# Kernel tuning notes

Measured on AMD Instinct MI355X. Metric: run time of the kernel, lower is better.

The kernel has to match this reference:

```python
import jax, jax.numpy as jnp
import numpy as np

D = 128  # embed dim

def linear(x, W, b):
    return x @ W.T + b

def mha1(x, w_in, b_in, w_out, b_out):
    # Single-head MultiheadAttention, x: (S, B, D), seq-first like torch.nn.MultiheadAttention
    q, k, v = jnp.split(x @ w_in.T + b_in, 3, axis=-1)
    scores = jnp.einsum('sbd,tbd->bst', q, k) / jnp.sqrt(jnp.asarray(D, x.dtype))
    att = jax.nn.softmax(scores, axis=-1)
    o = jnp.einsum('bst,tbd->sbd', att, v)
    return o @ w_out.T + b_out

def setup_inputs() -> dict:
    key = jax.random.key(0)
    ks = iter(jax.random.split(key, 32))
    def p(shape, scale=0.02):
        return (jax.random.normal(next(ks), shape, dtype=jnp.float32) * scale)
    B, S, F = 8, 2048, 3584
    inp = {
        'x': jax.random.normal(next(ks), (B, S, F), dtype=jnp.float32),
        'place_W': p((128, 2048)), 'place_b': p((128,)),
        'cast_W': p((128, 512)), 'cast_b': p((128,)),
        'action_W': p((128, 512)), 'action_b': p((128,)),
        'audio_W': p((128, 512)), 'audio_b': p((128,)),
        'e_W': p((128, 512)), 'e_b': p((128,)),
        'la_win': p((3 * D, D)), 'la_bin': p((3 * D,)),
        'la_wout': p((D, D)), 'la_bout': p((D,)),
        'be_W': p((128, 256)), 'be_b': p((128,)),
        'ba_win': p((3 * D, D)), 'ba_bin': p((3 * D,)),
        'ba_wout': p((D, D)), 'ba_bout': p((D,)),
        'bp_W': p((1, 128)), 'bp_b': p((1,)),
    }
    return inp

def reference(x, place_W, place_b, cast_W, cast_b, action_W, action_b,
              audio_W, audio_b, e_W, e_b, la_win, la_bin, la_wout, la_bout,
              be_W, be_b, ba_win, ba_bin, ba_wout, ba_bout, bp_W, bp_b):
    # --- forward_embeddings ---
    place = jax.nn.relu(linear(x[:, :, :2048], place_W, place_b))
    cast = jax.nn.relu(linear(x[:, :, 2048:2560], cast_W, cast_b))
    action = jax.nn.relu(linear(x[:, :, 2560:3072], action_W, action_b))
    audio = jax.nn.relu(linear(x[:, :, 3072:3584], audio_W, audio_b))
    feats = jnp.concatenate((place, cast, action, audio), axis=2)  # (B,S,512)
    e = jax.nn.relu(linear(feats, e_W, e_b))  # (B,S,128)
    e = jnp.transpose(e, (1, 0, 2))  # (S,B,128) seq-first
    e = mha1(e, la_win, la_bin, la_wout, la_bout)
    # --- forward_segmentation (single-pass prefix/suffix means) ---
    S = e.shape[0]
    csum = jnp.cumsum(e, axis=0)  # (S,B,D)
    total = csum[-1]
    i = jnp.arange(1, S, dtype=e.dtype)[:, None, None]
    left = csum[:-1] / i                       # mean of e[:i]
    right = (total[None] - csum[:-1]) / (S - i)  # mean of e[i:]
    cat = jnp.concatenate((left, right), axis=-1)  # (S-1,B,256)
    b = jax.nn.relu(linear(cat, be_W, be_b))
    b = mha1(b, ba_win, ba_bin, ba_wout, ba_bout)
    b = jax.nn.sigmoid(linear(b, bp_W, bp_b))[..., 0]  # (S-1,B)
    return (e, b)
```

## Files before the change

### kernel.cpp

```cpp
#include <hip/hip_runtime.h>
#include <hip/hip_bf16.h>
#include <math.h>
#include <stdint.h>


#define DEV static __device__ __forceinline__

typedef __attribute__((ext_vector_type(8))) short bf16x8;
typedef __attribute__((ext_vector_type(4))) float f32x4;

DEV uint32_t pk2bf(float a, float b) {
  __hip_bfloat162 h = __float22bfloat162_rn(make_float2(a, b));
  return *(uint32_t*)&h;
}
DEV uint2 cvt4(float4 f) {
  return make_uint2(pk2bf(f.x, f.y), pk2bf(f.z, f.w));
}
DEV uint16_t bf1(float a) { return (uint16_t)(pk2bf(a, 0.f) & 0xffffu); }
DEV float frombf(uint16_t h) {
  union { uint32_t u; float f; } v; v.u = ((uint32_t)h) << 16; return v.f;
}

#define WAIT_VM0()  __asm__ volatile("s_waitcnt vmcnt(0)" ::: "memory")
#define WAIT_LGKM0() __asm__ volatile("s_waitcnt lgkmcnt(0)" ::: "memory")
#define RAW_BARRIER() __builtin_amdgcn_s_barrier()

#define OFF_PW      0u
#define OFF_CW      262144u
#define OFF_AW      327680u
#define OFF_UW      393216u
#define OFF_EW      458752u
#define OFF_LAWIN   524288u
#define OFF_LAWOUT  573440u
#define OFF_BEW     589824u
#define OFF_BAWIN   622592u
#define OFF_BAWOUT  671744u
#define OFF_END     688128u

struct WPtrs { const float* p[10]; };

__global__ __launch_bounds__(256) void pack_weights(WPtrs wp, uint16_t* __restrict__ WB)
{
  const uint32_t off[11] = {OFF_PW, OFF_CW, OFF_AW, OFF_UW, OFF_EW, OFF_LAWIN,
                            OFF_LAWOUT, OFF_BEW, OFF_BAWIN, OFF_BAWOUT, OFF_END};
  uint32_t h = (blockIdx.x * 256u + threadIdx.x) * 4u;
  if (h >= OFF_END) return;
  int s = 0;
  while (h >= off[s + 1]) ++s;
  float4 f = *(const float4*)(wp.p[s] + (h - off[s]));
  *(uint2*)(WB + h) = cvt4(f);
}

template<bool ABF, bool OBF, bool RELU, bool REMAP>
__global__ __launch_bounds__(256) void gemm64(
    const void* __restrict__ Ap, int lda,
    const uint16_t* __restrict__ Wb,
    const float* __restrict__ bias,
    void* __restrict__ Cp, int ldc,
    int M, int K)
{
  __shared__ __align__(16) uint16_t As[64 * 72];
  __shared__ __align__(16) uint16_t Ws[128 * 72];

  const int t  = threadIdx.x;
  const int m0 = blockIdx.x * 64;
  const int n0 = blockIdx.y * 128;
  const int w  = t >> 6, l = t & 63;
  const int ln = l & 15, qd = l >> 4;

  f32x4 acc[4][2];
#pragma unroll
  for (int i = 0; i < 4; ++i) { acc[i][0] = (f32x4){0,0,0,0}; acc[i][1] = (f32x4){0,0,0,0}; }

  const int rr = t >> 4;
  const int cl = (t & 15) * 4;
  const int r8 = t >> 3;
  const int c8 = (t & 7) * 8;

  float4 a32[4];
  bf16x8 a16[2];
  bf16x8 wreg[4];

  auto loadA = [&](int k0) {
    if (ABF) {
      const uint16_t* A = (const uint16_t*)Ap;
#pragma unroll
      for (int i = 0; i < 2; ++i) {
        int m = m0 + r8 + 32 * i;
        int mc = m < M ? m : M - 1;
        a16[i] = *(const bf16x8*)(A + (size_t)mc * lda + k0 + c8);
      }
    } else {
      const float* A = (const float*)Ap;
#pragma unroll
      for (int i = 0; i < 4; ++i) {
        int m = m0 + rr + 16 * i;
        int mc = m < M ? m : M - 1;
        a32[i] = *(const float4*)(A + (size_t)mc * lda + k0 + cl);
      }
    }
#pragma unroll
    for (int i = 0; i < 4; ++i) {
      int n = r8 + 32 * i;
      wreg[i] = *(const bf16x8*)(Wb + (size_t)(n0 + n) * K + k0 + c8);
    }
  };
  auto writeLDS = [&]() {
    if (ABF) {
#pragma unroll
      for (int i = 0; i < 2; ++i)
        *(bf16x8*)(As + (size_t)(r8 + 32 * i) * 72 + c8) = a16[i];
    } else {
#pragma unroll
      for (int i = 0; i < 4; ++i)
        *(uint2*)(As + (size_t)(rr + 16 * i) * 72 + cl) = cvt4(a32[i]);
    }
#pragma unroll
    for (int i = 0; i < 4; ++i)
      *(bf16x8*)(Ws + (size_t)(r8 + 32 * i) * 72 + c8) = wreg[i];
  };

  loadA(0);
  for (int k0 = 0; k0 < K; k0 += 64) {
    WAIT_VM0();
    writeLDS();
    WAIT_LGKM0();
    RAW_BARRIER();
    if (k0 + 64 < K) loadA(k0 + 64);
#pragma unroll
    for (int ks = 0; ks < 2; ++ks) {
      bf16x8 af[4], bfr[2];
#pragma unroll
      for (int mf = 0; mf < 4; ++mf)
        af[mf] = *(const bf16x8*)(As + (size_t)(mf * 16 + ln) * 72 + ks * 32 + qd * 8);
#pragma unroll
      for (int nf = 0; nf < 2; ++nf)
        bfr[nf] = *(const bf16x8*)(Ws + (size_t)(w * 32 + nf * 16 + ln) * 72 + ks * 32 + qd * 8);
#pragma unroll
      for (int mf = 0; mf < 4; ++mf)
#pragma unroll
        for (int nf = 0; nf < 2; ++nf)
          acc[mf][nf] = __builtin_amdgcn_mfma_f32_16x16x32_bf16(af[mf], bfr[nf], acc[mf][nf], 0, 0, 0);
    }
    RAW_BARRIER();
  }

#pragma unroll
  for (int mf = 0; mf < 4; ++mf) {
#pragma unroll
    for (int r = 0; r < 4; ++r) {
      int m = m0 + mf * 16 + qd * 4 + r;
      if (m < M) {
        size_t ro = REMAP ? (size_t)((m & 2047) * 8 + (m >> 11)) : (size_t)m;
#pragma unroll
        for (int nf = 0; nf < 2; ++nf) {
          int n = n0 + w * 32 + nf * 16 + ln;
          float v = acc[mf][nf][r] + bias[n];
          if (RELU) v = fmaxf(v, 0.f);
          if (OBF) ((uint16_t*)Cp)[ro * (size_t)ldc + n] = bf1(v);
          else     ((float*)Cp)[ro * (size_t)ldc + n] = v;
        }
      }
    }
  }
}

__global__ __launch_bounds__(256) void gemm_feats64(
    const float* __restrict__ x, const uint16_t* __restrict__ WB,
    const float* __restrict__ pb, const float* __restrict__ cb,
    const float* __restrict__ ab, const float* __restrict__ ub,
    uint16_t* __restrict__ feats)
{
  __shared__ __align__(16) uint16_t As[64 * 72];
  __shared__ __align__(16) uint16_t Ws[128 * 72];

  const int seg = blockIdx.y;
  const uint16_t* Wb; const float* bias; int kbase, Kseg;
  if (seg == 0)      { Wb = WB + OFF_PW; bias = pb; kbase = 0;    Kseg = 2048; }
  else if (seg == 1) { Wb = WB + OFF_CW; bias = cb; kbase = 2048; Kseg = 512; }
  else if (seg == 2) { Wb = WB + OFF_AW; bias = ab; kbase = 2560; Kseg = 512; }
  else               { Wb = WB + OFF_UW; bias = ub; kbase = 3072; Kseg = 512; }

  const int t  = threadIdx.x;
  const int m0 = blockIdx.x * 64;
  const int w  = t >> 6, l = t & 63;
  const int ln = l & 15, qd = l >> 4;

  f32x4 acc[4][2];
#pragma unroll
  for (int i = 0; i < 4; ++i) { acc[i][0] = (f32x4){0,0,0,0}; acc[i][1] = (f32x4){0,0,0,0}; }

  const int rr = t >> 4;
  const int cl = (t & 15) * 4;
  const int r8 = t >> 3;
  const int c8 = (t & 7) * 8;

  float4 a32[4];
  bf16x8 wreg[4];

  auto loadA = [&](int k0) {
#pragma unroll
    for (int i = 0; i < 4; ++i) {
      int m = m0 + rr + 16 * i;
      a32[i] = *(const float4*)(x + (size_t)m * 3584 + kbase + k0 + cl);
    }
#pragma unroll
    for (int i = 0; i < 4; ++i) {
      int n = r8 + 32 * i;
      wreg[i] = *(const bf16x8*)(Wb + (size_t)n * Kseg + k0 + c8);
    }
  };

  loadA(0);
  for (int k0 = 0; k0 < Kseg; k0 += 64) {
    WAIT_VM0();
#pragma unroll
    for (int i = 0; i < 4; ++i)
      *(uint2*)(As + (size_t)(rr + 16 * i) * 72 + cl) = cvt4(a32[i]);
#pragma unroll
    for (int i = 0; i < 4; ++i)
      *(bf16x8*)(Ws + (size_t)(r8 + 32 * i) * 72 + c8) = wreg[i];
    WAIT_LGKM0();
    RAW_BARRIER();
    if (k0 + 64 < Kseg) loadA(k0 + 64);
#pragma unroll
    for (int ks = 0; ks < 2; ++ks) {
      bf16x8 af[4], bfr[2];
#pragma unroll
      for (int mf = 0; mf < 4; ++mf)
        af[mf] = *(const bf16x8*)(As + (size_t)(mf * 16 + ln) * 72 + ks * 32 + qd * 8);
#pragma unroll
      for (int nf = 0; nf < 2; ++nf)
        bfr[nf] = *(const bf16x8*)(Ws + (size_t)(w * 32 + nf * 16 + ln) * 72 + ks * 32 + qd * 8);
#pragma unroll
      for (int mf = 0; mf < 4; ++mf)
#pragma unroll
        for (int nf = 0; nf < 2; ++nf)
          acc[mf][nf] = __builtin_amdgcn_mfma_f32_16x16x32_bf16(af[mf], bfr[nf], acc[mf][nf], 0, 0, 0);
    }
    RAW_BARRIER();
  }

#pragma unroll
  for (int mf = 0; mf < 4; ++mf) {
#pragma unroll
    for (int r = 0; r < 4; ++r) {
      int m = m0 + mf * 16 + qd * 4 + r;
#pragma unroll
      for (int nf = 0; nf < 2; ++nf) {
        int n = w * 32 + nf * 16 + ln;
        float v = fmaxf(acc[mf][nf][r] + bias[n], 0.f);
        feats[(size_t)m * 512 + seg * 128 + n] = bf1(v);
      }
    }
  }
}

__global__ __launch_bounds__(256) void gemm_becat64(
    const float* __restrict__ csum, const float* __restrict__ part,
    const uint16_t* __restrict__ Wb, const float* __restrict__ bias,
    uint16_t* __restrict__ C)
{
  __shared__ __align__(16) uint16_t As[64 * 72];
  __shared__ __align__(16) uint16_t Ws[128 * 72];

  const int M = 16376, K = 256;
  const int t  = threadIdx.x;
  const int m0 = blockIdx.x * 64;
  const int w  = t >> 6, l = t & 63;
  const int ln = l & 15, qd = l >> 4;

  f32x4 acc[4][2];
#pragma unroll
  for (int i = 0; i < 4; ++i) { acc[i][0] = (f32x4){0,0,0,0}; acc[i][1] = (f32x4){0,0,0,0}; }

  const int rr = t >> 4;
  const int cl = (t & 15) * 4;
  const int r8 = t >> 3;
  const int c8 = (t & 7) * 8;

  for (int k0 = 0; k0 < K; k0 += 64) {
    __syncthreads();
#pragma unroll
    for (int i = 0; i < 4; ++i) {
      int m = m0 + rr + 16 * i;
      int mc = m < M ? m : M - 1;
      int j = mc >> 3, bb = mc & 7;
      int kk = k0 + cl;
      float4 f;
      if (kk < 128) {
        float4 v = *(const float4*)(csum + (size_t)mc * 128 + kk);
        float4 p = *(const float4*)(part + (size_t)(bb * 64 + (j >> 5)) * 128 + kk);
        float s = 1.f / (float)(j + 1);
        f = make_float4((v.x + p.x) * s, (v.y + p.y) * s,
                        (v.z + p.z) * s, (v.w + p.w) * s);
      } else {
        int d = kk - 128;
        float4 c0 = *(const float4*)(csum + (size_t)mc * 128 + d);
        float4 p0 = *(const float4*)(part + (size_t)(bb * 64 + (j >> 5)) * 128 + d);
        float4 ct = *(const float4*)(csum + (size_t)(16376 + bb) * 128 + d);
        float4 pt = *(const float4*)(part + (size_t)(bb * 64 + 63) * 128 + d);
        float s = 1.f / (float)(2047 - j);
        f = make_float4(((ct.x + pt.x) - (c0.x + p0.x)) * s,
                        ((ct.y + pt.y) - (c0.y + p0.y)) * s,
                        ((ct.z + pt.z) - (c0.z + p0.z)) * s,
                        ((ct.w + pt.w) - (c0.w + p0.w)) * s);
      }
      *(uint2*)(As + (size_t)(rr + 16 * i) * 72 + cl) = cvt4(f);
    }
#pragma unroll
    for (int i = 0; i < 4; ++i) {
      int n = r8 + 32 * i;
      *(bf16x8*)(Ws + (size_t)n * 72 + c8) =
          *(const bf16x8*)(Wb + (size_t)n * K + k0 + c8);
    }
    __syncthreads();
#pragma unroll
    for (int ks = 0; ks < 2; ++ks) {
      bf16x8 af[4], bfr[2];
#pragma unroll
      for (int mf = 0; mf < 4; ++mf)
        af[mf] = *(const bf16x8*)(As + (size_t)(mf * 16 + ln) * 72 + ks * 32 + qd * 8);
#pragma unroll
      for (int nf = 0; nf < 2; ++nf)
        bfr[nf] = *(const bf16x8*)(Ws + (size_t)(w * 32 + nf * 16 + ln) * 72 + ks * 32 + qd * 8);
#pragma unroll
      for (int mf = 0; mf < 4; ++mf)
#pragma unroll
        for (int nf = 0; nf < 2; ++nf)
          acc[mf][nf] = __builtin_amdgcn_mfma_f32_16x16x32_bf16(af[mf], bfr[nf], acc[mf][nf], 0, 0, 0);
    }
  }

#pragma unroll
  for (int mf = 0; mf < 4; ++mf) {
#pragma unroll
    for (int r = 0; r < 4; ++r) {
      int m = m0 + mf * 16 + qd * 4 + r;
      if (m < M) {
#pragma unroll
        for (int nf = 0; nf < 2; ++nf) {
          int n = w * 32 + nf * 16 + ln;
          C[(size_t)m * 128 + n] = bf1(fmaxf(acc[mf][nf][r] + bias[n], 0.f));
        }
      }
    }
  }
}

__global__ __launch_bounds__(256) void vpack(
    const uint16_t* __restrict__ proj, uint16_t* __restrict__ Vtb, int Slen)
{
  __shared__ __align__(16) uint16_t Vs[64][136];

  const int kt = blockIdx.x, b = blockIdx.y, t = threadIdx.x;
  const int sl = t >> 2, cg = (t & 3) * 32;
  const int s  = kt * 64 + sl;
  const int valid = s < Slen;
  const int sc2 = valid ? s : Slen - 1;
  const uint16_t* src = proj + ((size_t)sc2 * 8 + b) * 384 + 256 + cg;
#pragma unroll
  for (int i = 0; i < 4; ++i) {
    bf16x8 v;
    if (valid) v = *(const bf16x8*)(src + i * 8);
    else       v = (bf16x8){0,0,0,0,0,0,0,0};
    *(bf16x8*)(&Vs[sl][cg + i * 8]) = v;
  }
  __syncthreads();
  const int d = t >> 1, hh = t & 1;
  uint32_t wv[16];
#pragma unroll
  for (int i = 0; i < 16; ++i) {
    int K = 32 * hh + 16 * ((i >> 1) & 1) + 4 * ((i >> 2) & 3) + 2 * (i & 1);
    wv[i] = (uint32_t)Vs[K][d] | ((uint32_t)Vs[K + 1][d] << 16);
  }
  uint16_t* dv = Vtb + (((size_t)b * 32 + kt) * 128 + d) * 64 + hh * 32;
#pragma unroll
  for (int i = 0; i < 4; ++i)
    *(uint4*)(dv + i * 8) = *(uint4*)(&wv[i * 4]);
}

__global__ __launch_bounds__(256, 3) void attn_split3(
    const uint16_t* __restrict__ proj, const uint16_t* __restrict__ Vtb,
    float* __restrict__ Opart, float* __restrict__ ml, int Slen)
{
  __shared__ __align__(16) uint16_t KsL[64 * 136];
  __shared__ __align__(16) uint16_t VtL[128 * 72];

  const int t  = threadIdx.x;
  const int b  = blockIdx.y;
  const int q0 = blockIdx.x * 64;
  const int split = blockIdx.z;
  const int kbeg = split * 704;
  const int kend = (split == 2) ? Slen : kbeg + 704;
  const int w  = t >> 6;
  const int l  = t & 63;
  const int ln = l & 15;
  const int qd = l >> 4;
  const float scl = 0.08838834764831845f;

  const int kkey = t >> 2, kcg = (t & 3) * 32;
  const int vd   = t >> 1, vh  = (t & 1) * 32;

  bf16x8 qf[4];
  {
    int qrow = q0 + w * 16 + ln;
    int qc = qrow < Slen ? qrow : Slen - 1;
    const uint16_t* qp = proj + ((size_t)qc * 8 + b) * 384 + qd * 8;
#pragma unroll
    for (int ks = 0; ks < 4; ++ks) {
      union { bf16x8 v; uint16_t h[8]; uint32_t u[4]; } in, out;
      in.v = *(const bf16x8*)(qp + ks * 32);
#pragma unroll
      for (int j = 0; j < 4; ++j)
        out.u[j] = pk2bf(frombf(in.h[2 * j]) * scl, frombf(in.h[2 * j + 1]) * scl);
      qf[ks] = out.v;
    }
  }

  f32x4 oacc[8];
#pragma unroll
  for (int i = 0; i < 8; ++i) oacc[i] = (f32x4){0.f, 0.f, 0.f, 0.f};
  float mrow = -INFINITY;
  float lrow = 0.f;

  const int ntiles = (kend - kbeg + 63) >> 6;

  bf16x8 kreg[4], vreg[4];
  auto loadTile = [&](int kt) {
    int kg = kbeg + kt * 64 + kkey;
    int kc = kg < Slen ? kg : Slen - 1;
    const uint16_t* ksrc = proj + ((size_t)kc * 8 + b) * 384 + 128 + kcg;
#pragma unroll
    for (int i = 0; i < 4; ++i) kreg[i] = *(const bf16x8*)(ksrc + i * 8);
    const int tile = 11 * split + kt;
    const uint16_t* vsrc = Vtb + (((size_t)b * 32 + tile) * 128 + vd) * 64 + vh;
#pragma unroll
    for (int i = 0; i < 4; ++i) vreg[i] = *(const bf16x8*)(vsrc + i * 8);
  };

  loadTile(0);
  for (int kt = 0; kt < ntiles; ++kt) {
    WAIT_VM0();
    {
      uint16_t* kdst = KsL + kkey * 136 + kcg;
#pragma unroll
      for (int i = 0; i < 4; ++i) *(bf16x8*)(kdst + i * 8) = kreg[i];
      uint16_t* vdst = VtL + vd * 72 + vh;
#pragma unroll
      for (int i = 0; i < 4; ++i) *(bf16x8*)(vdst + i * 8) = vreg[i];
    }
    WAIT_LGKM0();
    RAW_BARRIER();
    if (kt + 1 < ntiles) loadTile(kt + 1);

    float sc[4][4];
    __builtin_amdgcn_s_setprio(1);
#pragma unroll
    for (int nf = 0; nf < 4; ++nf) {
      f32x4 acc = (f32x4){0.f, 0.f, 0.f, 0.f};
#pragma unroll
      for (int ks = 0; ks < 4; ++ks) {
        bf16x8 kf = *(const bf16x8*)(KsL + (size_t)(nf * 16 + ln) * 136 + ks * 32 + qd * 8);
        acc = __builtin_amdgcn_mfma_f32_16x16x32_bf16(kf, qf[ks], acc, 0, 0, 0);
      }
      int keyb = kbeg + kt * 64 + nf * 16 + qd * 4;
#pragma unroll
      for (int r = 0; r < 4; ++r)
        sc[nf][r] = (keyb + r < kend) ? acc[r] : -1e30f;
    }
    __builtin_amdgcn_s_setprio(0);

    float mx = sc[0][0];
#pragma unroll
    for (int nf = 0; nf < 4; ++nf)
#pragma unroll
      for (int r = 0; r < 4; ++r) mx = fmaxf(mx, sc[nf][r]);
    mx = fmaxf(mx, __shfl_xor(mx, 16));
    mx = fmaxf(mx, __shfl_xor(mx, 32));
    float mNew = fmaxf(mrow, mx);

    float ps = 0.f;
#pragma unroll
    for (int nf = 0; nf < 4; ++nf) {
      float p0 = __expf(sc[nf][0] - mNew);
      float p1 = __expf(sc[nf][1] - mNew);
      float p2 = __expf(sc[nf][2] - mNew);
      float p3 = __expf(sc[nf][3] - mNew);
      sc[nf][0] = p0; sc[nf][1] = p1; sc[nf][2] = p2; sc[nf][3] = p3;
      ps += (p0 + p1) + (p2 + p3);
    }
    ps += __shfl_xor(ps, 16);
    ps += __shfl_xor(ps, 32);

    float alpha = __expf(mrow - mNew);
    mrow = mNew;
    lrow = lrow * alpha + ps;

    float alphaR[4];
#pragma unroll
    for (int r = 0; r < 4; ++r)
      alphaR[r] = __shfl(alpha, (l & 48) | (qd * 4 + r));
#pragma unroll
    for (int no = 0; no < 8; ++no) {
#pragma unroll
      for (int r = 0; r < 4; ++r) oacc[no][r] *= alphaR[r];
    }

    union { bf16x8 v; uint32_t u[4]; } pa0, pa1;
#pragma unroll
    for (int i = 0; i < 4; ++i) {
      pa0.u[i] = pk2bf(sc[(i >> 1)][(i & 1) * 2],     sc[(i >> 1)][(i & 1) * 2 + 1]);
      pa1.u[i] = pk2bf(sc[2 + (i >> 1)][(i & 1) * 2], sc[2 + (i >> 1)][(i & 1) * 2 + 1]);
    }
    __builtin_amdgcn_s_setprio(1);
#pragma unroll
    for (int no = 0; no < 8; ++no) {
      bf16x8 vf = *(const bf16x8*)(VtL + (size_t)(no * 16 + ln) * 72 + qd * 8);
      oacc[no] = __builtin_amdgcn_mfma_f32_16x16x32_bf16(pa0.v, vf, oacc[no], 0, 0, 0);
    }
#pragma unroll
    for (int no = 0; no < 8; ++no) {
      bf16x8 vf = *(const bf16x8*)(VtL + (size_t)(no * 16 + ln) * 72 + 32 + qd * 8);
      oacc[no] = __builtin_amdgcn_mfma_f32_16x16x32_bf16(pa1.v, vf, oacc[no], 0, 0, 0);
    }
    __builtin_amdgcn_s_setprio(0);
    RAW_BARRIER();
  }

#pragma unroll
  for (int r = 0; r < 4; ++r) {
    int qg = q0 + w * 16 + qd * 4 + r;
    if (qg < Slen) {
      size_t row = (size_t)qg * 8 + b;
      float* dst = Opart + ((size_t)split * 16384 + row) * 128 + ln;
#pragma unroll
      for (int no = 0; no < 8; ++no) dst[no * 16] = oacc[no][r];
    }
  }
  {
    int qg = q0 + w * 16 + ln;
    if (qd == 0 && qg < Slen) {
      size_t row = (size_t)qg * 8 + b;
      ml[((size_t)split * 16384 + row) * 2 + 0] = mrow;
      ml[((size_t)split * 16384 + row) * 2 + 1] = lrow;
    }
  }
}

template<bool HEAD>
__global__ __launch_bounds__(256) void gemm_attc64(
    const float* __restrict__ Opart, const float* __restrict__ ml,
    const uint16_t* __restrict__ Wb,
    const float* __restrict__ bias,
    const float* __restrict__ bpW, const float* __restrict__ bpb,
    float* __restrict__ out, int M)
{
  __shared__ __align__(16) uint16_t As[64 * 72];
  __shared__ __align__(16) uint16_t Ws[128 * 72];
  __shared__ float RW[64][4];
  __shared__ float Ct[HEAD ? 64 : 1][133];

  const int K = 128;
  const int t  = threadIdx.x;
  const int m0 = blockIdx.x * 64;
  const int w  = t >> 6, l = t & 63;
  const int ln = l & 15, qd = l >> 4;

  if (t < 64) {
    int m = m0 + t;
    int mc = m < M ? m : M - 1;
    float m0v = ml[(size_t)mc * 2],                 l0 = ml[(size_t)mc * 2 + 1];
    float m1v = ml[((size_t)16384 + mc) * 2],       l1 = ml[((size_t)16384 + mc) * 2 + 1];
    float m2v = ml[((size_t)32768 + mc) * 2],       l2 = ml[((size_t)32768 + mc) * 2 + 1];
    float Mx = fmaxf(fmaxf(m0v, m1v), m2v);
    float w0 = __expf(m0v - Mx), w1 = __expf(m1v - Mx), w2 = __expf(m2v - Mx);
    RW[t][0] = w0; RW[t][1] = w1; RW[t][2] = w2;
    RW[t][3] = 1.f / (l0 * w0 + l1 * w1 + l2 * w2);
  }
  __syncthreads();

  f32x4 acc[4][2];
#pragma unroll
  for (int i = 0; i < 4; ++i) { acc[i][0] = (f32x4){0,0,0,0}; acc[i][1] = (f32x4){0,0,0,0}; }

  const int rr = t >> 4;
  const int cl = (t & 15) * 4;
  const int r8 = t >> 3;
  const int c8 = (t & 7) * 8;

  float4 ra[4], rc[4], re[4];
  bf16x8 wreg[4];

  auto loadA = [&](int k0) {
#pragma unroll
    for (int i = 0; i < 4; ++i) {
      int m = m0 + rr + 16 * i;
      int mc = m < M ? m : M - 1;
      int kk = k0 + cl;
      ra[i] = *(const float4*)(Opart + (size_t)mc * 128 + kk);
      rc[i] = *(const float4*)(Opart + ((size_t)16384 + mc) * 128 + kk);
      re[i] = *(const float4*)(Opart + ((size_t)32768 + mc) * 128 + kk);
    }
#pragma unroll
    for (int i = 0; i < 4; ++i) {
      int n = r8 + 32 * i;
      wreg[i] = *(const bf16x8*)(Wb + (size_t)n * K + k0 + c8);
    }
  };

  loadA(0);
  for (int k0 = 0; k0 < K; k0 += 64) {
    WAIT_VM0();
#pragma unroll
    for (int i = 0; i < 4; ++i) {
      int rl = rr + 16 * i;
      float w0 = RW[rl][0], w1 = RW[rl][1], w2 = RW[rl][2], inv = RW[rl][3];
      float4 f = make_float4((ra[i].x * w0 + rc[i].x * w1 + re[i].x * w2) * inv,
                             (ra[i].y * w0 + rc[i].y * w1 + re[i].y * w2) * inv,
                             (ra[i].z * w0 + rc[i].z * w1 + re[i].z * w2) * inv,
                             (ra[i].w * w0 + rc[i].w * w1 + re[i].w * w2) * inv);
      *(uint2*)(As + (size_t)rl * 72 + cl) = cvt4(f);
    }
#pragma unroll
    for (int i = 0; i < 4; ++i)
      *(bf16x8*)(Ws + (size_t)(r8 + 32 * i) * 72 + c8) = wreg[i];
    WAIT_LGKM0();
    RAW_BARRIER();
    if (k0 + 64 < K) loadA(k0 + 64);
#pragma unroll
    for (int ks = 0; ks < 2; ++ks) {
      bf16x8 af[4], bfr[2];
#pragma unroll
      for (int mf = 0; mf < 4; ++mf)
        af[mf] = *(const bf16x8*)(As + (size_t)(mf * 16 + ln) * 72 + ks * 32 + qd * 8);
#pragma unroll
      for (int nf = 0; nf < 2; ++nf)
        bfr[nf] = *(const bf16x8*)(Ws + (size_t)(w * 32 + nf * 16 + ln) * 72 + ks * 32 + qd * 8);
#pragma unroll
      for (int mf = 0; mf < 4; ++mf)
#pragma unroll
        for (int nf = 0; nf < 2; ++nf)
          acc[mf][nf] = __builtin_amdgcn_mfma_f32_16x16x32_bf16(af[mf], bfr[nf], acc[mf][nf], 0, 0, 0);
    }
    RAW_BARRIER();
  }

  if (HEAD) {
    __syncthreads();
#pragma unroll
    for (int mf = 0; mf < 4; ++mf) {
#pragma unroll
      for (int r = 0; r < 4; ++r) {
        int rowL = mf * 16 + qd * 4 + r;
#pragma unroll
        for (int nf = 0; nf < 2; ++nf) {
          int n = w * 32 + nf * 16 + ln;
          Ct[rowL][n] = acc[mf][nf][r] + bias[n];
        }
      }
    }
    __syncthreads();
    int row = t >> 2, qg = t & 3;
    int m = m0 + row;
    float p = 0.f;
#pragma unroll
    for (int j = 0; j < 32; ++j) {
      int c = qg + j * 4;
      p += Ct[row][c] * bpW[c];
    }
    p += __shfl_xor(p, 1);
    p += __shfl_xor(p, 2);
    if (qg == 0 && m < M)
      out[m] = 1.f / (1.f + __expf(-(p + bpb[0])));
  } else {
#pragma unroll
    for (int mf = 0; mf < 4; ++mf) {
#pragma unroll
      for (int r = 0; r < 4; ++r) {
        int m = m0 + mf * 16 + qd * 4 + r;
        if (m < M) {
#pragma unroll
          for (int nf = 0; nf < 2; ++nf) {
            int n = w * 32 + nf * 16 + ln;
            out[(size_t)m * 128 + n] = acc[mf][nf][r] + bias[n];
          }
        }
      }
    }
  }
}

__global__ void cumsum_p1(const float* __restrict__ e, float* __restrict__ csum,
                          float* __restrict__ part)
{
  int chunk = blockIdx.x, b = blockIdx.y, d = threadIdx.x;
  float run = 0.f;
  int s0 = chunk * 32;
  for (int s = 0; s < 32; ++s) {
    size_t idx = ((size_t)(s0 + s) * 8 + b) * 128 + d;
    run += e[idx];
    csum[idx] = run;
  }
  part[(b * 64 + chunk) * 128 + d] = run;
}

__global__ void cumsum_p2(float* __restrict__ part)
{
  int b = blockIdx.x, d = threadIdx.x;
  float run = 0.f;
  for (int c = 0; c < 64; ++c) {
    float v = part[(b * 64 + c) * 128 + d];
    part[(b * 64 + c) * 128 + d] = run;
    run += v;
  }
}

extern "C" void kernel_launch(void* const* d_in, const int* in_sizes, int n_in,
                              void* d_out, int out_size, void* d_ws, size_t ws_size,
                              hipStream_t stream)
{
  const float* x       = (const float*)d_in[0];
  const float* pW      = (const float*)d_in[1];
  const float* pb      = (const float*)d_in[2];
  const float* cW      = (const float*)d_in[3];
  const float* cb      = (const float*)d_in[4];
  const float* aW      = (const float*)d_in[5];
  const float* ab      = (const float*)d_in[6];
  const float* uW      = (const float*)d_in[7];
  const float* ub      = (const float*)d_in[8];
  const float* eW      = (const float*)d_in[9];
  const float* eb      = (const float*)d_in[10];
  const float* la_win  = (const float*)d_in[11];
  const float* la_bin  = (const float*)d_in[12];
  const float* la_wout = (const float*)d_in[13];
  const float* la_bout = (const float*)d_in[14];
  const float* beW     = (const float*)d_in[15];
  const float* beb     = (const float*)d_in[16];
  const float* ba_win  = (const float*)d_in[17];
  const float* ba_bin  = (const float*)d_in[18];
  const float* ba_wout = (const float*)d_in[19];
  const float* ba_bout = (const float*)d_in[20];
  const float* bpW     = (const float*)d_in[21];
  const float* bpb     = (const float*)d_in[22];

  float* ws   = (float*)d_ws;
  float* outF = (float*)d_out;

  uint16_t* WB  = (uint16_t*)ws;
  float* base   = ws + 344064;
  uint16_t* featsB = (uint16_t*)base;
  float* csumB  = base;
  float* partB  = base + 2097152;
  uint16_t* eB  = (uint16_t*)(base + 4194304);
  uint16_t* projB = (uint16_t*)(base + 5242880);
  uint16_t* VtbB  = (uint16_t*)(base + 8388608);
  float* OpartB = base + 9437184;
  float* mlB    = base + 15728640;

  WPtrs wp;
  wp.p[0] = pW; wp.p[1] = cW; wp.p[2] = aW; wp.p[3] = uW; wp.p[4] = eW;
  wp.p[5] = la_win; wp.p[6] = la_wout; wp.p[7] = beW; wp.p[8] = ba_win; wp.p[9] = ba_wout;
  pack_weights<<<dim3(672), 256, 0, stream>>>(wp, WB);

  gemm_feats64<<<dim3(256, 4), 256, 0, stream>>>(x, WB, pb, cb, ab, ub, featsB);
  gemm64<true, true, true, true><<<dim3(256, 1), 256, 0, stream>>>(
      featsB, 512, WB + OFF_EW, eb, eB, 128, 16384, 512);
  gemm64<true, true, false, false><<<dim3(256, 3), 256, 0, stream>>>(
      eB, 128, WB + OFF_LAWIN, la_bin, projB, 384, 16384, 128);
  vpack<<<dim3(32, 8), 256, 0, stream>>>(projB, VtbB, 2048);
  attn_split3<<<dim3(32, 8, 3), 256, 0, stream>>>(projB, VtbB, OpartB, mlB, 2048);
  gemm_attc64<false><<<dim3(256), 256, 0, stream>>>(
      OpartB, mlB, WB + OFF_LAWOUT, la_bout, nullptr, nullptr, outF, 16384);
  cumsum_p1<<<dim3(64, 8), 128, 0, stream>>>(outF, csumB, partB);
  cumsum_p2<<<dim3(8), 128, 0, stream>>>(partB);
  gemm_becat64<<<dim3(256), 256, 0, stream>>>(csumB, partB, WB + OFF_BEW, beb, eB);
  gemm64<true, true, false, false><<<dim3(256, 3), 256, 0, stream>>>(
      eB, 128, WB + OFF_BAWIN, ba_bin, projB, 384, 16376, 128);
  vpack<<<dim3(32, 8), 256, 0, stream>>>(projB, VtbB, 2047);
  attn_split3<<<dim3(32, 8, 3), 256, 0, stream>>>(projB, VtbB, OpartB, mlB, 2047);
  gemm_attc64<true><<<dim3(256), 256, 0, stream>>>(
      OpartB, mlB, WB + OFF_BAWOUT, ba_bout, bpW, bpb, outF + 2097152, 16376);
}
```

Baseline: 517.1 us.

## Read K and V fragments directly from global memory in split attention kernel

Removes the shared-memory staging of K and V tiles, the register prefetch pipeline and the block barriers from the split attention kernel. Each wave now loads its MFMA operands straight from global memory, relying on L1/L2 caching, because all four waves of a block read the same K/V tile. This drops LDS traffic and synchronisation and frees occupancy from the LDS limit. It gives up explicit prefetch overlap and makes each wave issue redundant global loads, which may expose memory latency.

```diff
diff --git a/kernel.cpp b/kernel.cpp
--- a/kernel.cpp
+++ b/kernel.cpp
@@ -380,13 +380,10 @@
     *(uint4*)(dv + i * 8) = *(uint4*)(&wv[i * 4]);
 }
 
-__global__ __launch_bounds__(256, 3) void attn_split3(
+__global__ __launch_bounds__(256) void attn_split3(
     const uint16_t* __restrict__ proj, const uint16_t* __restrict__ Vtb,
     float* __restrict__ Opart, float* __restrict__ ml, int Slen)
 {
-  __shared__ __align__(16) uint16_t KsL[64 * 136];
-  __shared__ __align__(16) uint16_t VtL[128 * 72];
-
   const int t  = threadIdx.x;
   const int b  = blockIdx.y;
   const int q0 = blockIdx.x * 64;
@@ -399,9 +396,6 @@
   const int qd = l >> 4;
   const float scl = 0.08838834764831845f;
 
-  const int kkey = t >> 2, kcg = (t & 3) * 32;
-  const int vd   = t >> 1, vh  = (t & 1) * 32;
-
   bf16x8 qf[4];
   {
     int qrow = q0 + w * 16 + ln;
@@ -426,45 +420,23 @@
 
   const int ntiles = (kend - kbeg + 63) >> 6;
 
-  bf16x8 kreg[4], vreg[4];
-  auto loadTile = [&](int kt) {
-    int kg = kbeg + kt * 64 + kkey;
-    int kc = kg < Slen ? kg : Slen - 1;
-    const uint16_t* ksrc = proj + ((size_t)kc * 8 + b) * 384 + 128 + kcg;
-#pragma unroll
-    for (int i = 0; i < 4; ++i) kreg[i] = *(const bf16x8*)(ksrc + i * 8);
-    const int tile = 11 * split + kt;
-    const uint16_t* vsrc = Vtb + (((size_t)b * 32 + tile) * 128 + vd) * 64 + vh;
-#pragma unroll
-    for (int i = 0; i < 4; ++i) vreg[i] = *(const bf16x8*)(vsrc + i * 8);
-  };
-
-  loadTile(0);
   for (int kt = 0; kt < ntiles; ++kt) {
-    WAIT_VM0();
-    {
-      uint16_t* kdst = KsL + kkey * 136 + kcg;
-#pragma unroll
-      for (int i = 0; i < 4; ++i) *(bf16x8*)(kdst + i * 8) = kreg[i];
-      uint16_t* vdst = VtL + vd * 72 + vh;
-#pragma unroll
-      for (int i = 0; i < 4; ++i) *(bf16x8*)(vdst + i * 8) = vreg[i];
-    }
-    WAIT_LGKM0();
-    RAW_BARRIER();
-    if (kt + 1 < ntiles) loadTile(kt + 1);
+    const int key0 = kbeg + kt * 64;
 
     float sc[4][4];
     __builtin_amdgcn_s_setprio(1);
 #pragma unroll
     for (int nf = 0; nf < 4; ++nf) {
+      int key = key0 + nf * 16 + ln;
+      int kc = key < Slen ? key : Slen - 1;
+      const uint16_t* kp = proj + ((size_t)kc * 8 + b) * 384 + 128 + qd * 8;
       f32x4 acc = (f32x4){0.f, 0.f, 0.f, 0.f};
 #pragma unroll
       for (int ks = 0; ks < 4; ++ks) {
-        bf16x8 kf = *(const bf16x8*)(KsL + (size_t)(nf * 16 + ln) * 136 + ks * 32 + qd * 8);
+        bf16x8 kf = *(const bf16x8*)(kp + ks * 32);
         acc = __builtin_amdgcn_mfma_f32_16x16x32_bf16(kf, qf[ks], acc, 0, 0, 0);
       }
-      int keyb = kbeg + kt * 64 + nf * 16 + qd * 4;
+      int keyb = key0 + nf * 16 + qd * 4;
 #pragma unroll
       for (int r = 0; r < 4; ++r)
         sc[nf][r] = (keyb + r < kend) ? acc[r] : -1e30f;
@@ -513,19 +485,20 @@
       pa0.u[i] = pk2bf(sc[(i >> 1)][(i & 1) * 2],     sc[(i >> 1)][(i & 1) * 2 + 1]);
       pa1.u[i] = pk2bf(sc[2 + (i >> 1)][(i & 1) * 2], sc[2 + (i >> 1)][(i & 1) * 2 + 1]);
     }
+
+    const uint16_t* vbase = Vtb + (((size_t)b * 32 + 11 * split + kt) * 128) * 64;
     __builtin_amdgcn_s_setprio(1);
 #pragma unroll
     for (int no = 0; no < 8; ++no) {
-      bf16x8 vf = *(const bf16x8*)(VtL + (size_t)(no * 16 + ln) * 72 + qd * 8);
+      bf16x8 vf = *(const bf16x8*)(vbase + (size_t)(no * 16 + ln) * 64 + qd * 8);
       oacc[no] = __builtin_amdgcn_mfma_f32_16x16x32_bf16(pa0.v, vf, oacc[no], 0, 0, 0);
     }
 #pragma unroll
     for (int no = 0; no < 8; ++no) {
-      bf16x8 vf = *(const bf16x8*)(VtL + (size_t)(no * 16 + ln) * 72 + 32 + qd * 8);
+      bf16x8 vf = *(const bf16x8*)(vbase + (size_t)(no * 16 + ln) * 64 + 32 + qd * 8);
       oacc[no] = __builtin_amdgcn_mfma_f32_16x16x32_bf16(pa1.v, vf, oacc[no], 0, 0, 0);
     }
     __builtin_amdgcn_s_setprio(0);
-    RAW_BARRIER();
   }
 
 #pragma unroll
```

Result: slower. 677.4 us (+31.0%).
